# Performance work log

Hardware: AMD Instinct MI355X
Metric: run time of the kernel (lower is better)

The kernel has to match this reference:

```python
import jax, jax.numpy as jnp
import numpy as np

N = 100000   # nodes
E = 1600000  # edges
IN = 768     # in_dim
H = 128      # hidden_dim
G = 64       # graphs per batch


def setup_inputs() -> dict:
    key = jax.random.key(0)
    ks = jax.random.split(key, 9)
    x = jax.random.normal(ks[0], (N, IN), jnp.float32)
    edge_index = jax.random.randint(ks[1], (2, E), 0, N, dtype=jnp.int64)
    batch = jnp.sort(jax.random.randint(ks[2], (N,), 0, G, dtype=jnp.int64))
    W1 = jax.random.normal(ks[3], (IN, H), jnp.float32) / np.float32(np.sqrt(IN))
    b1 = jax.random.normal(ks[4], (H,), jnp.float32) * 0.01
    W2 = jax.random.normal(ks[5], (H, H), jnp.float32) / np.float32(np.sqrt(H))
    b2 = jax.random.normal(ks[6], (H,), jnp.float32) * 0.01
    Wh = jax.random.normal(ks[7], (H, 2), jnp.float32) / np.float32(np.sqrt(H))
    bh = jax.random.normal(ks[8], (2,), jnp.float32) * 0.01
    return dict(x=x, edge_index=edge_index, batch=batch, W1=W1, b1=b1,
                W2=W2, b2=b2, Wh=Wh, bh=bh, num_graphs=G)


def gcn_conv(x, src, dst, W, b, n):
    # PyG GCNConv default: add self-loops (already in src/dst), symmetric norm.
    deg = jax.ops.segment_sum(jnp.ones_like(dst, x.dtype), dst, num_segments=n)
    dis = jnp.where(deg > 0, jax.lax.rsqrt(deg), jnp.zeros_like(deg))
    h = x @ W                                   # [n, out]
    norm = (dis[src] * dis[dst])[:, None]       # [E+n, 1]
    out = jax.ops.segment_sum(h[src] * norm, dst, num_segments=n)
    return out + b


def reference(x, edge_index, batch, W1, b1, W2, b2, Wh, bh, num_graphs):
    n = x.shape[0]
    loop = jnp.arange(n, dtype=edge_index.dtype)
    src = jnp.concatenate([edge_index[0], loop])
    dst = jnp.concatenate([edge_index[1], loop])
    h = jax.nn.relu(gcn_conv(x, src, dst, W1, b1, n))   # dropout = eval identity
    h = jax.nn.relu(gcn_conv(h, src, dst, W2, b2, n))
    summed = jax.ops.segment_sum(h, batch, num_segments=num_graphs)
    counts = jax.ops.segment_sum(jnp.ones((n, 1), h.dtype), batch, num_segments=num_graphs)
    emb = summed / jnp.maximum(counts, 1.0)             # global_mean_pool
    return emb @ Wh + bh
```

## Files before the change

### kernel.cpp

```cpp
#include <hip/hip_runtime.h>
#include <hip/hip_bf16.h>
#include <hip/hip_fp16.h>

static constexpr int N_NODES  = 100000;
static constexpr int N_EDGES  = 1600000;
static constexpr int DIM_IN   = 768;
static constexpr int DIM_H    = 128;
static constexpr int N_GRAPHS = 64;
static constexpr int NB_SCAN  = (N_NODES + 255) / 256;

typedef __attribute__((ext_vector_type(8))) _Float16 half8;
typedef __attribute__((ext_vector_type(4))) float f32x4;

__global__ void k_indeg(const int* __restrict__ edst, int* __restrict__ indeg) {
    int e = blockIdx.x * 256 + threadIdx.x;
    if (e < N_EDGES) atomicAdd(&indeg[edst[e]], 1);
}

__global__ void k_convW(const float* __restrict__ W1, const float* __restrict__ W2,
                        _Float16* __restrict__ W1t, _Float16* __restrict__ W2t) {
    int i = blockIdx.x * 256 + threadIdx.x;
    const int total1 = DIM_IN * DIM_H;
    if (i < total1) {
        int k = i >> 7, n = i & 127;
        W1t[(size_t)n * DIM_IN + k] = (_Float16)W1[i];
    } else if (i < total1 + DIM_H * DIM_H) {
        int j = i - total1;
        int k = j >> 7, n = j & 127;
        W2t[(size_t)n * DIM_H + k] = (_Float16)W2[j];
    }
}

__global__ void k_scan1(const int* __restrict__ indeg, int* __restrict__ rp,
                        int* __restrict__ bsum, float* __restrict__ dis) {
    __shared__ int s[256];
    int t = threadIdx.x;
    int i = blockIdx.x * 256 + t;
    int v = (i < N_NODES) ? indeg[i] : 0;
    s[t] = v;
    __syncthreads();
    for (int off = 1; off < 256; off <<= 1) {
        int x = (t >= off) ? s[t - off] : 0;
        __syncthreads();
        s[t] += x;
        __syncthreads();
    }
    if (i < N_NODES) {
        rp[i] = s[t] - v;
        dis[i] = rsqrtf((float)v + 1.0f);
    }
    if (t == 255) bsum[blockIdx.x] = s[255];
}

__global__ void k_scan2(int* __restrict__ bsum, const int* __restrict__ batch,
                        int* __restrict__ gstart) {
    __shared__ int s[512];
    int t = threadIdx.x;
    int v = (t < NB_SCAN) ? bsum[t] : 0;
    s[t] = v;
    __syncthreads();
    for (int off = 1; off < 512; off <<= 1) {
        int x = (t >= off) ? s[t - off] : 0;
        __syncthreads();
        s[t] += x;
        __syncthreads();
    }
    if (t < NB_SCAN) bsum[t] = s[t] - v;
    if (t <= N_GRAPHS) {
        int lo = 0, hi = N_NODES;
        while (lo < hi) {
            int mid = (lo + hi) >> 1;
            if (batch[mid] < t) lo = mid + 1; else hi = mid;
        }
        gstart[t] = lo;
    }
}

__global__ void k_scatter(const int* __restrict__ esrc, const int* __restrict__ edst,
                          const int* __restrict__ rp, const int* __restrict__ bsum,
                          const float* __restrict__ dis,
                          int* __restrict__ cursor, uint2* __restrict__ csrw) {
    int e = blockIdx.x * 256 + threadIdx.x;
    if (e >= N_EDGES) return;
    int d = edst[e];
    int sv = esrc[e];
    int pos = atomicAdd(&cursor[d], 1);
    uint2 val;
    val.x = (uint)sv;
    val.y = __float_as_uint(dis[sv]);
    csrw[rp[d] + bsum[d >> 8] + pos] = val;
}

#define LDSTR 40

template<int K, bool AFP32>
__global__ __launch_bounds__(256) void k_gemm_mfma(const void* __restrict__ Av,
                                                   const _Float16* __restrict__ Wt,
                                                   _Float16* __restrict__ C,
                                                   int nrows) {
    __shared__ ushort As[128 * LDSTR];
    __shared__ ushort Bs[128 * LDSTR];

    const int t = threadIdx.x;
    const int row0 = blockIdx.x * 128;
    const int srow = t >> 1;
    const int skoff = (t & 1) * 16;
    const int l = t & 63;
    const int wv = t >> 6;
    const int wm = wv >> 1, wn = wv & 1;
    const int lr = l & 15;
    const int lk = (l >> 4) * 8;

    f32x4 acc[4][4];
    const f32x4 zero = {0.f, 0.f, 0.f, 0.f};
    #pragma unroll
    for (int m = 0; m < 4; ++m)
        #pragma unroll
        for (int n = 0; n < 4; ++n) acc[m][n] = zero;

    for (int k0 = 0; k0 < K; k0 += 32) {
        if (AFP32) {
            union { _Float16 h[16]; uint4 q[2]; } cv;
            float f[16];
            if (row0 + srow < nrows) {
                const float4* Ap = (const float4*)((const float*)Av +
                    (size_t)(row0 + srow) * K + k0 + skoff);
                *(float4*)&f[0]  = Ap[0];
                *(float4*)&f[4]  = Ap[1];
                *(float4*)&f[8]  = Ap[2];
                *(float4*)&f[12] = Ap[3];
            } else {
                #pragma unroll
                for (int i = 0; i < 16; ++i) f[i] = 0.f;
            }
            #pragma unroll
            for (int i = 0; i < 16; ++i) cv.h[i] = (_Float16)f[i];
            *(uint4*)&As[srow * LDSTR + skoff]     = cv.q[0];
            *(uint4*)&As[srow * LDSTR + skoff + 8] = cv.q[1];
        } else {
            uint4 q0 = {0, 0, 0, 0}, q1 = {0, 0, 0, 0};
            if (row0 + srow < nrows) {
                const uint4* Ap = (const uint4*)((const _Float16*)Av +
                    (size_t)(row0 + srow) * K + k0 + skoff);
                q0 = Ap[0]; q1 = Ap[1];
            }
            *(uint4*)&As[srow * LDSTR + skoff]     = q0;
            *(uint4*)&As[srow * LDSTR + skoff + 8] = q1;
        }
        {
            const uint4* Wp = (const uint4*)(Wt + (size_t)srow * K + k0 + skoff);
            *(uint4*)&Bs[srow * LDSTR + skoff]     = Wp[0];
            *(uint4*)&Bs[srow * LDSTR + skoff + 8] = Wp[1];
        }
        __syncthreads();

        half8 a[4], b[4];
        #pragma unroll
        for (int m = 0; m < 4; ++m)
            a[m] = *(const half8*)&As[(wm * 64 + m * 16 + lr) * LDSTR + lk];
        #pragma unroll
        for (int n = 0; n < 4; ++n)
            b[n] = *(const half8*)&Bs[(wn * 64 + n * 16 + lr) * LDSTR + lk];
        #pragma unroll
        for (int m = 0; m < 4; ++m)
            #pragma unroll
            for (int n = 0; n < 4; ++n)
                acc[m][n] = __builtin_amdgcn_mfma_f32_16x16x32_f16(a[m], b[n], acc[m][n], 0, 0, 0);
        __syncthreads();
    }

    #pragma unroll
    for (int m = 0; m < 4; ++m) {
        #pragma unroll
        for (int n = 0; n < 4; ++n) {
            int col = wn * 64 + n * 16 + lr;
            #pragma unroll
            for (int j = 0; j < 4; ++j) {
                int row = row0 + wm * 64 + m * 16 + (l >> 4) * 4 + j;
                if (row < nrows)
                    C[(size_t)row * DIM_H + col] = (_Float16)acc[m][n][j];
            }
        }
    }
}

__device__ __forceinline__ void acc8(uint4 u, float w, float* a) {
    __half2 h0 = *(__half2*)&u.x;
    __half2 h1 = *(__half2*)&u.y;
    __half2 h2 = *(__half2*)&u.z;
    __half2 h3 = *(__half2*)&u.w;
    a[0] += __low2float(h0) * w; a[1] += __high2float(h0) * w;
    a[2] += __low2float(h1) * w; a[3] += __high2float(h1) * w;
    a[4] += __low2float(h2) * w; a[5] += __high2float(h2) * w;
    a[6] += __low2float(h3) * w; a[7] += __high2float(h3) * w;
}

__global__ __launch_bounds__(256) void k_agg(const _Float16* __restrict__ hin,
                                             const uint2* __restrict__ csrw,
                                             const int* __restrict__ rp,
                                             const int* __restrict__ bsum,
                                             const int* __restrict__ indeg,
                                             const float* __restrict__ dis,
                                             const float* __restrict__ bias,
                                             _Float16* __restrict__ hout) {
    int node = (blockIdx.x * 256 + threadIdx.x) >> 6;
    int lane = threadIdx.x & 63;
    if (node >= N_NODES) return;
    int q  = lane >> 4;
    int cl = lane & 15;
    float di = dis[node];
    int beg = rp[node] + bsum[node >> 8];
    int cnt = indeg[node];

    float a[8] = {0.f, 0.f, 0.f, 0.f, 0.f, 0.f, 0.f, 0.f};

    {
        uint s; float w;
        if (q == 0)             { s = (uint)node; w = di * di; }
        else if (q - 1 < cnt)   { uint2 p = csrw[beg + q - 1]; s = p.x; w = __uint_as_float(p.y) * di; }
        else                    { s = (uint)node; w = 0.f; }
        uint4 u = ((const uint4*)(hin + (size_t)s * DIM_H))[cl];
        acc8(u, w, a);
    }
    const uint2* cp = csrw + beg + 3;
    int m = cnt - 3;
    int i = 0;
    for (; i + 8 <= m; i += 8) {
        uint2 p0 = cp[i + q];
        uint2 p1 = cp[i + 4 + q];
        float w0 = __uint_as_float(p0.y) * di;
        float w1 = __uint_as_float(p1.y) * di;
        uint4 u0 = ((const uint4*)(hin + (size_t)p0.x * DIM_H))[cl];
        uint4 u1 = ((const uint4*)(hin + (size_t)p1.x * DIM_H))[cl];
        acc8(u0, w0, a);
        acc8(u1, w1, a);
    }
    for (; i < m; i += 4) {
        int idx = i + q;
        uint s; float w;
        if (idx < m) { uint2 p = cp[idx]; s = p.x; w = __uint_as_float(p.y) * di; }
        else         { s = (uint)node;    w = 0.f; }
        uint4 u = ((const uint4*)(hin + (size_t)s * DIM_H))[cl];
        acc8(u, w, a);
    }

    #pragma unroll
    for (int j = 0; j < 8; ++j) {
        a[j] += __shfl_xor(a[j], 16);
        a[j] += __shfl_xor(a[j], 32);
    }

    if (q == 0) {
        float4 b0 = ((const float4*)bias)[cl * 2];
        float4 b1 = ((const float4*)bias)[cl * 2 + 1];
        __half2 h0 = __floats2half2_rn(fmaxf(a[0] + b0.x, 0.f), fmaxf(a[1] + b0.y, 0.f));
        __half2 h1 = __floats2half2_rn(fmaxf(a[2] + b0.z, 0.f), fmaxf(a[3] + b0.w, 0.f));
        __half2 h2 = __floats2half2_rn(fmaxf(a[4] + b1.x, 0.f), fmaxf(a[5] + b1.y, 0.f));
        __half2 h3 = __floats2half2_rn(fmaxf(a[6] + b1.z, 0.f), fmaxf(a[7] + b1.w, 0.f));
        uint4 o;
        o.x = *(uint*)&h0; o.y = *(uint*)&h1; o.z = *(uint*)&h2; o.w = *(uint*)&h3;
        ((uint4*)(hout + (size_t)node * DIM_H))[cl] = o;
    }
}

#define PSPLIT 8
__global__ __launch_bounds__(256) void k_pool(const _Float16* __restrict__ h,
                                              const int* __restrict__ gstart,
                                              float* __restrict__ pooled2) {
    int g  = blockIdx.x >> 3;
    int sp = blockIdx.x & 7;
    int r0 = gstart[g], r1 = gstart[g + 1];
    int count = r1 - r0;
    int chunk = (count + PSPLIT - 1) / PSPLIT;
    int aS = r0 + sp * chunk;
    int bE = min(aS + chunk, r1);
    int c  = threadIdx.x & 63;
    int rr = threadIdx.x >> 6;
    float s0a = 0.f, s1a = 0.f, s0b = 0.f, s1b = 0.f;
    int r = aS + rr;
    for (; r + 4 < bE; r += 8) {
        uint ua = ((const uint*)(h + (size_t)r * DIM_H))[c];
        uint ub = ((const uint*)(h + (size_t)(r + 4) * DIM_H))[c];
        __half2 ha = *(__half2*)&ua;
        __half2 hb = *(__half2*)&ub;
        s0a += __low2float(ha); s1a += __high2float(ha);
        s0b += __low2float(hb); s1b += __high2float(hb);
    }
    if (r < bE) {
        uint ua = ((const uint*)(h + (size_t)r * DIM_H))[c];
        __half2 ha = *(__half2*)&ua;
        s0a += __low2float(ha); s1a += __high2float(ha);
    }
    float s0 = s0a + s0b, s1 = s1a + s1b;
    __shared__ float sm0[4][64], sm1[4][64];
    sm0[rr][c] = s0; sm1[rr][c] = s1;
    __syncthreads();
    if (rr == 0) {
        float v0 = sm0[0][c] + sm0[1][c] + sm0[2][c] + sm0[3][c];
        float v1 = sm1[0][c] + sm1[1][c] + sm1[2][c] + sm1[3][c];
        float* dst = pooled2 + (size_t)(g * PSPLIT + sp) * DIM_H;
        dst[2 * c]     = v0;
        dst[2 * c + 1] = v1;
    }
}

__global__ __launch_bounds__(128) void k_head(const float* __restrict__ pooled2,
                                              const int* __restrict__ gstart,
                                              const float* __restrict__ Wh,
                                              const float* __restrict__ bh,
                                              float* __restrict__ out) {
    int g = blockIdx.x;
    int c = threadIdx.x;
    float s = 0.f;
    #pragma unroll
    for (int sp = 0; sp < PSPLIT; ++sp)
        s += pooled2[(size_t)(g * PSPLIT + sp) * DIM_H + c];
    float cntg = (float)(gstart[g + 1] - gstart[g]);
    float e = s / fmaxf(cntg, 1.0f);
    __shared__ float s0[128], s1[128];
    s0[c] = e * Wh[c * 2 + 0];
    s1[c] = e * Wh[c * 2 + 1];
    __syncthreads();
    for (int off = 64; off > 0; off >>= 1) {
        if (c < off) { s0[c] += s0[c + off]; s1[c] += s1[c + off]; }
        __syncthreads();
    }
    if (c == 0) {
        out[g * 2 + 0] = s0[0] + bh[0];
        out[g * 2 + 1] = s1[0] + bh[1];
    }
}

extern "C" void kernel_launch(void* const* d_in, const int* in_sizes, int n_in,
                              void* d_out, int out_size, void* d_ws, size_t ws_size,
                              hipStream_t stream) {
    const float* x    = (const float*)d_in[0];
    const int*   esrc = (const int*)d_in[1];
    const int*   edst = esrc + N_EDGES;
    const int*   batch= (const int*)d_in[2];
    const float* W1   = (const float*)d_in[3];
    const float* b1   = (const float*)d_in[4];
    const float* W2   = (const float*)d_in[5];
    const float* b2   = (const float*)d_in[6];
    const float* Wh   = (const float*)d_in[7];
    const float* bh   = (const float*)d_in[8];
    float* out = (float*)d_out;

    char* ws = (char*)d_ws;
    size_t off = 0;
    auto alloc = [&](size_t bytes) {
        void* p = ws + off;
        off += (bytes + 255) & ~(size_t)255;
        return p;
    };
    _Float16* bufZ   = (_Float16*)alloc((size_t)N_NODES * DIM_H * 2);
    _Float16* bufH   = (_Float16*)alloc((size_t)N_NODES * DIM_H * 2);
    float*    dis    = (float*)alloc((size_t)N_NODES * 4);
    int*      deg2   = (int*)  alloc((size_t)2 * N_NODES * 4);
    int*      indeg  = deg2;
    int*      cursor = deg2 + N_NODES;
    int*      rp     = (int*)  alloc((size_t)N_NODES * 4);
    uint2*    csrw   = (uint2*)alloc((size_t)N_EDGES * 8);
    int*      bsum   = (int*)  alloc(512 * 4);
    float*    pooled2= (float*)alloc((size_t)N_GRAPHS * PSPLIT * DIM_H * 4);
    int*      gstart = (int*)  alloc((N_GRAPHS + 1) * 4);
    _Float16* W1t    = (_Float16*)alloc((size_t)DIM_IN * DIM_H * 2);
    _Float16* W2t    = (_Float16*)alloc((size_t)DIM_H * DIM_H * 2);

    hipMemsetAsync(deg2, 0, (size_t)2 * N_NODES * 4, stream);

    int convblocks = (DIM_IN * DIM_H + DIM_H * DIM_H + 255) / 256;
    k_convW  <<<convblocks, 256, 0, stream>>>(W1, W2, W1t, W2t);

    k_indeg  <<<(N_EDGES + 255) / 256, 256, 0, stream>>>(edst, indeg);
    k_scan1  <<<NB_SCAN, 256, 0, stream>>>(indeg, rp, bsum, dis);
    k_scan2  <<<1, 512, 0, stream>>>(bsum, batch, gstart);
    k_scatter<<<(N_EDGES + 255) / 256, 256, 0, stream>>>(esrc, edst, rp, bsum, dis, cursor, csrw);

    int gblocks = (N_NODES + 127) / 128;
    k_gemm_mfma<DIM_IN, true ><<<gblocks, 256, 0, stream>>>(x,    W1t, bufZ, N_NODES);
    k_agg<<<(N_NODES + 3) / 4, 256, 0, stream>>>(bufZ, csrw, rp, bsum, indeg, dis, b1, bufH);
    k_gemm_mfma<DIM_H,  false><<<gblocks, 256, 0, stream>>>(bufH, W2t, bufZ, N_NODES);
    k_agg<<<(N_NODES + 3) / 4, 256, 0, stream>>>(bufZ, csrw, rp, bsum, indeg, dis, b2, bufH);

    k_pool<<<N_GRAPHS * PSPLIT, 256, 0, stream>>>(bufH, gstart, pooled2);
    k_head<<<N_GRAPHS, 128, 0, stream>>>(pooled2, gstart, Wh, bh, out);
}
```

Before: 441.5 us.

## Fuse edge scatter into first GEMM launch and double GEMM K-tile

The CSR scatter kernel is folded into the first GEMM launch as extra trailing blocks, so the memory-bound scatter can run alongside the compute-bound GEMM instead of in a separate launch. The GEMM K tile grows from 32 to 64, which halves the number of barrier pairs per tile and increases the loads in flight per thread. In exchange, LDS use doubles and register pressure rises from the 32-float staging buffer. The scatter blocks also take slots in the same grid.

After: 417.1 us. 5.5% less time.

```diff
diff --git a/kernel.cpp b/kernel.cpp
--- a/kernel.cpp
+++ b/kernel.cpp
@@ -76,40 +76,49 @@
     }
 }
 
-__global__ void k_scatter(const int* __restrict__ esrc, const int* __restrict__ edst,
-                          const int* __restrict__ rp, const int* __restrict__ bsum,
-                          const float* __restrict__ dis,
-                          int* __restrict__ cursor, uint2* __restrict__ csrw) {
-    int e = blockIdx.x * 256 + threadIdx.x;
-    if (e >= N_EDGES) return;
-    int d = edst[e];
-    int sv = esrc[e];
-    int pos = atomicAdd(&cursor[d], 1);
-    uint2 val;
-    val.x = (uint)sv;
-    val.y = __float_as_uint(dis[sv]);
-    csrw[rp[d] + bsum[d >> 8] + pos] = val;
-}
-
-#define LDSTR 40
-
-template<int K, bool AFP32>
+#define BKV 64
+#define LDSTR 72
+
+template<int K, bool AFP32, bool FUSE_SCATTER>
 __global__ __launch_bounds__(256) void k_gemm_mfma(const void* __restrict__ Av,
                                                    const _Float16* __restrict__ Wt,
                                                    _Float16* __restrict__ C,
-                                                   int nrows) {
+                                                   int nrows,
+                                                   const int* __restrict__ esrc,
+                                                   const int* __restrict__ edst,
+                                                   const int* __restrict__ rp,
+                                                   const int* __restrict__ bsum,
+                                                   const float* __restrict__ dis,
+                                                   int* __restrict__ cursor,
+                                                   uint2* __restrict__ csrw,
+                                                   int gemm_blocks) {
     __shared__ ushort As[128 * LDSTR];
     __shared__ ushort Bs[128 * LDSTR];
+
+    if (FUSE_SCATTER && (int)blockIdx.x >= gemm_blocks) {
+        int e = (blockIdx.x - gemm_blocks) * 256 + threadIdx.x;
+        if (e < N_EDGES) {
+            int d = edst[e];
+            int sv = esrc[e];
+            int pos = atomicAdd(&cursor[d], 1);
+            uint2 val;
+            val.x = (uint)sv;
+            val.y = __float_as_uint(dis[sv]);
+            csrw[rp[d] + bsum[d >> 8] + pos] = val;
+        }
+        return;
+    }
 
     const int t = threadIdx.x;
     const int row0 = blockIdx.x * 128;
     const int srow = t >> 1;
-    const int skoff = (t & 1) * 16;
+    const int scol = (t & 1) * 32;
     const int l = t & 63;
     const int wv = t >> 6;
     const int wm = wv >> 1, wn = wv & 1;
     const int lr = l & 15;
     const int lk = (l >> 4) * 8;
+    const bool arow_ok = (row0 + srow < nrows);
 
     f32x4 acc[4][4];
     const f32x4 zero = {0.f, 0.f, 0.f, 0.f};
@@ -118,54 +127,59 @@
         #pragma unroll
         for (int n = 0; n < 4; ++n) acc[m][n] = zero;
 
-    for (int k0 = 0; k0 < K; k0 += 32) {
+    for (int k0 = 0; k0 < K; k0 += BKV) {
         if (AFP32) {
-            union { _Float16 h[16]; uint4 q[2]; } cv;
-            float f[16];
-            if (row0 + srow < nrows) {
+            union { _Float16 h[32]; uint4 q[4]; } cv;
+            float f[32];
+            if (arow_ok) {
                 const float4* Ap = (const float4*)((const float*)Av +
-                    (size_t)(row0 + srow) * K + k0 + skoff);
-                *(float4*)&f[0]  = Ap[0];
-                *(float4*)&f[4]  = Ap[1];
-                *(float4*)&f[8]  = Ap[2];
-                *(float4*)&f[12] = Ap[3];
+                    (size_t)(row0 + srow) * K + k0 + scol);
+                #pragma unroll
+                for (int i = 0; i < 8; ++i) *(float4*)&f[4 * i] = Ap[i];
             } else {
                 #pragma unroll
-                for (int i = 0; i < 16; ++i) f[i] = 0.f;
+                for (int i = 0; i < 32; ++i) f[i] = 0.f;
             }
             #pragma unroll
-            for (int i = 0; i < 16; ++i) cv.h[i] = (_Float16)f[i];
-            *(uint4*)&As[srow * LDSTR + skoff]     = cv.q[0];
-            *(uint4*)&As[srow * LDSTR + skoff + 8] = cv.q[1];
+            for (int i = 0; i < 32; ++i) cv.h[i] = (_Float16)f[i];
+            #pragma unroll
+            for (int i = 0; i < 4; ++i)
+                *(uint4*)&As[srow * LDSTR + scol + 8 * i] = cv.q[i];
         } else {
-            uint4 q0 = {0, 0, 0, 0}, q1 = {0, 0, 0, 0};
-            if (row0 + srow < nrows) {
+            uint4 q[4] = {{0,0,0,0},{0,0,0,0},{0,0,0,0},{0,0,0,0}};
+            if (arow_ok) {
                 const uint4* Ap = (const uint4*)((const _Float16*)Av +
-                    (size_t)(row0 + srow) * K + k0 + skoff);
-                q0 = Ap[0]; q1 = Ap[1];
+                    (size_t)(row0 + srow) * K + k0 + scol);
+                #pragma unroll
+                for (int i = 0; i < 4; ++i) q[i] = Ap[i];
             }
-            *(uint4*)&As[srow * LDSTR + skoff]     = q0;
-            *(uint4*)&As[srow * LDSTR + skoff + 8] = q1;
+            #pragma unroll
+            for (int i = 0; i < 4; ++i)
+                *(uint4*)&As[srow * LDSTR + scol + 8 * i] = q[i];
         }
         {
-            const uint4* Wp = (const uint4*)(Wt + (size_t)srow * K + k0 + skoff);
-            *(uint4*)&Bs[srow * LDSTR + skoff]     = Wp[0];
-            *(uint4*)&Bs[srow * LDSTR + skoff + 8] = Wp[1];
-        }
-        __syncthreads();
-
-        half8 a[4], b[4];
+            const uint4* Wp = (const uint4*)(Wt + (size_t)srow * K + k0 + scol);
+            #pragma unroll
+            for (int i = 0; i < 4; ++i)
+                *(uint4*)&Bs[srow * LDSTR + scol + 8 * i] = Wp[i];
+        }
+        __syncthreads();
+
         #pragma unroll
-        for (int m = 0; m < 4; ++m)
-            a[m] = *(const half8*)&As[(wm * 64 + m * 16 + lr) * LDSTR + lk];
-        #pragma unroll
-        for (int n = 0; n < 4; ++n)
-            b[n] = *(const half8*)&Bs[(wn * 64 + n * 16 + lr) * LDSTR + lk];
-        #pragma unroll
-        for (int m = 0; m < 4; ++m)
+        for (int ks = 0; ks < BKV; ks += 32) {
+            half8 a[4], b[4];
+            #pragma unroll
+            for (int m = 0; m < 4; ++m)
+                a[m] = *(const half8*)&As[(wm * 64 + m * 16 + lr) * LDSTR + ks + lk];
             #pragma unroll
             for (int n = 0; n < 4; ++n)
-                acc[m][n] = __builtin_amdgcn_mfma_f32_16x16x32_f16(a[m], b[n], acc[m][n], 0, 0, 0);
+                b[n] = *(const half8*)&Bs[(wn * 64 + n * 16 + lr) * LDSTR + ks + lk];
+            #pragma unroll
+            for (int m = 0; m < 4; ++m)
+                #pragma unroll
+                for (int n = 0; n < 4; ++n)
+                    acc[m][n] = __builtin_amdgcn_mfma_f32_16x16x32_f16(a[m], b[n], acc[m][n], 0, 0, 0);
+        }
         __syncthreads();
     }
 
@@ -375,12 +389,14 @@
     k_indeg  <<<(N_EDGES + 255) / 256, 256, 0, stream>>>(edst, indeg);
     k_scan1  <<<NB_SCAN, 256, 0, stream>>>(indeg, rp, bsum, dis);
     k_scan2  <<<1, 512, 0, stream>>>(bsum, batch, gstart);
-    k_scatter<<<(N_EDGES + 255) / 256, 256, 0, stream>>>(esrc, edst, rp, bsum, dis, cursor, csrw);
 
     int gblocks = (N_NODES + 127) / 128;
-    k_gemm_mfma<DIM_IN, true ><<<gblocks, 256, 0, stream>>>(x,    W1t, bufZ, N_NODES);
+    int scblocks = (N_EDGES + 255) / 256;
+    k_gemm_mfma<DIM_IN, true, true><<<gblocks + scblocks, 256, 0, stream>>>(
+        x, W1t, bufZ, N_NODES, esrc, edst, rp, bsum, dis, cursor, csrw, gblocks);
     k_agg<<<(N_NODES + 3) / 4, 256, 0, stream>>>(bufZ, csrw, rp, bsum, indeg, dis, b1, bufH);
-    k_gemm_mfma<DIM_H,  false><<<gblocks, 256, 0, stream>>>(bufH, W2t, bufZ, N_NODES);
+    k_gemm_mfma<DIM_H, false, false><<<gblocks, 256, 0, stream>>>(
+        bufH, W2t, bufZ, N_NODES, nullptr, nullptr, nullptr, nullptr, nullptr, nullptr, nullptr, gblocks);
     k_agg<<<(N_NODES + 3) / 4, 256, 0, stream>>>(bufZ, csrw, rp, bsum, indeg, dis, b2, bufH);
 
     k_pool<<<N_GRAPHS * PSPLIT, 256, 0, stream>>>(bufH, gstart, pooled2);
```
